# Performance work log

Hardware: AMD Instinct MI355X
Metric: run time of the kernel (lower is better)

The kernel has to match this reference:

```python
import jax, jax.numpy as jnp
import numpy as np

N_EMBD = 1024
N_HEAD = 16
HEAD_DIM = N_EMBD // N_HEAD
B, T = 2, 2048


def setup_inputs() -> dict:
    key = jax.random.key(0)
    ks = jax.random.split(key, 9)
    s = 1.0 / np.sqrt(N_EMBD)
    return {
        "x": jax.random.normal(ks[0], (B, T, N_EMBD), dtype=jnp.float32),
        "Wq": jax.random.normal(ks[1], (N_EMBD, N_EMBD), dtype=jnp.float32) * s,
        "bq": jax.random.normal(ks[2], (N_EMBD,), dtype=jnp.float32) * s,
        "Wk": jax.random.normal(ks[3], (N_EMBD, N_EMBD), dtype=jnp.float32) * s,
        "bk": jax.random.normal(ks[4], (N_EMBD,), dtype=jnp.float32) * s,
        "Wv": jax.random.normal(ks[5], (N_EMBD, N_EMBD), dtype=jnp.float32) * s,
        "bv": jax.random.normal(ks[6], (N_EMBD,), dtype=jnp.float32) * s,
        "Wp": jax.random.normal(ks[7], (N_EMBD, N_EMBD), dtype=jnp.float32) * s,
        "bp": jax.random.normal(ks[8], (N_EMBD,), dtype=jnp.float32) * s,
    }


def reference(x, Wq, bq, Wk, bk, Wv, bv, Wp, bp):
    b, t, c = x.shape
    # torch Linear: y = x @ W.T + b
    def proj(W, bias):
        y = jnp.einsum('btc,oc->bto', x, W) + bias
        return y.reshape(b, t, N_HEAD, HEAD_DIM).transpose(0, 2, 1, 3)  # [B,H,T,D]

    q = proj(Wq, bq)
    k = proj(Wk, bk)
    v = proj(Wv, bv)

    scale = 1.0 / np.sqrt(HEAD_DIM).astype(np.float32)
    scores = jnp.einsum('bhqd,bhkd->bhqk', q, k) * scale  # [B,H,T,T]
    causal = jnp.tril(jnp.ones((t, t), dtype=bool))
    scores = jnp.where(causal[None, None], scores, jnp.float32(-jnp.inf))
    attn = jax.nn.softmax(scores, axis=-1)
    out = jnp.einsum('bhqk,bhkd->bhqd', attn, v)  # [B,H,T,D]
    out = out.transpose(0, 2, 1, 3).reshape(b, t, c)
    out = jnp.einsum('btc,oc->bto', out, Wp) + bp
    return out
```

## Files before the change

kernel.cpp:

```cpp
#include <hip/hip_runtime.h>
#include <hip/hip_bf16.h>

#define TT 2048
#define MM 4096

typedef __attribute__((ext_vector_type(8))) short bf16x8;
typedef __attribute__((ext_vector_type(4))) float f32x4;

__device__ inline short f2bf(float f){
  union { float f; unsigned u; } x; x.f = f;
  unsigned r = x.u + 0x7FFFu + ((x.u >> 16) & 1u);
  return (short)(r >> 16);
}
__device__ inline int pk2bf(float a, float b){
  __hip_bfloat162 h2 = __float22bfloat162_rn(make_float2(a, b));
  return *(int*)&h2;
}

__device__ inline void async16(const void* g, void* l){
  __builtin_amdgcn_global_load_lds((const __attribute__((address_space(1))) void*)g,
                                   (__attribute__((address_space(3))) void*)l, 16, 0, 0);
}

__global__ void cvt_all(const float* __restrict__ x,
                        const float* __restrict__ Wq, const float* __restrict__ Wk,
                        const float* __restrict__ Wv, const float* __restrict__ Wp,
                        short* __restrict__ xb, short* __restrict__ Wqb, short* __restrict__ Wkb,
                        short* __restrict__ Wvb, short* __restrict__ Wpb){
  int b = blockIdx.x;
  const float* in; short* out; int base;
  if (b < 4096)      { in = x;  out = xb;  base = b; }
  else if (b < 5120) { in = Wq; out = Wqb; base = b - 4096; }
  else if (b < 6144) { in = Wk; out = Wkb; base = b - 5120; }
  else if (b < 7168) { in = Wv; out = Wvb; base = b - 6144; }
  else               { in = Wp; out = Wpb; base = b - 7168; }
  int i = base * 256 + threadIdx.x;
  float4 v = ((const float4*)in)[i];
  short4 o;
  o.x = f2bf(v.x); o.y = f2bf(v.y); o.z = f2bf(v.z); o.w = f2bf(v.w);
  ((short4*)out)[i] = o;
}

__device__ inline void gemm_core(const short* __restrict__ A, const short* __restrict__ Wm,
                                 short* As, short* Bs, int m0, int n0,
                                 int tid, int wm, int wn, int quad, int lr,
                                 f32x4 acc[4][4])
{
  const int prow = tid >> 2, pcol = (tid & 3) << 3;
  const short* Ap0 = A  + (size_t)(m0 + prow) * 1024 + pcol;
  const short* Ap1 = A  + (size_t)(m0 + prow + 64) * 1024 + pcol;
  const short* Bp0 = Wm + (size_t)(n0 + prow) * 1024 + pcol;
  const short* Bp1 = Wm + (size_t)(n0 + prow + 64) * 1024 + pcol;
  for (int kt = 0; kt < 16; ++kt){
    const int kk = kt * 64;
#pragma unroll
    for (int pn = 0; pn < 2; ++pn){
      async16(Ap0 + kk + pn*32, As + pn*4096 + (size_t)tid * 8);
      async16(Ap1 + kk + pn*32, As + pn*4096 + (size_t)(tid + 256) * 8);
      async16(Bp0 + kk + pn*32, Bs + pn*4096 + (size_t)tid * 8);
      async16(Bp1 + kk + pn*32, Bs + pn*4096 + (size_t)(tid + 256) * 8);
    }
    __syncthreads();
#pragma unroll
    for (int ks = 0; ks < 2; ++ks){
      bf16x8 aF[4], bF[4];
#pragma unroll
      for (int mt = 0; mt < 4; ++mt) aF[mt] = *(const bf16x8*)(As + ks*4096 + (wm*64 + mt*16 + lr)*32 + quad*8);
#pragma unroll
      for (int nt = 0; nt < 4; ++nt) bF[nt] = *(const bf16x8*)(Bs + ks*4096 + (wn*64 + nt*16 + lr)*32 + quad*8);
#pragma unroll
      for (int mt = 0; mt < 4; ++mt)
#pragma unroll
        for (int nt = 0; nt < 4; ++nt)
          acc[mt][nt] = __builtin_amdgcn_mfma_f32_16x16x32_bf16(aF[mt], bF[nt], acc[mt][nt], 0, 0, 0);
    }
    __syncthreads();
  }
}

__launch_bounds__(256, 3)
__global__ void gemm_qkv(const short* __restrict__ A,
                         const short* __restrict__ W0, const short* __restrict__ W1, const short* __restrict__ W2,
                         const float* __restrict__ b0, const float* __restrict__ b1, const float* __restrict__ b2,
                         short* __restrict__ Qo, short* __restrict__ Ko, short* __restrict__ Vt)
{
  __shared__ __align__(16) short smem[16384];
  short* As = smem;
  short* Bs = smem + 8192;
  const int z = blockIdx.z;
  const short* Wm   = (z == 0) ? W0 : ((z == 1) ? W1 : W2);
  const float* bias = (z == 0) ? b0 : ((z == 1) ? b1 : b2);
  const int tid = threadIdx.x;
  const int lane = tid & 63, wave = tid >> 6;
  const int wm = wave >> 1, wn = wave & 1;
  const int quad = lane >> 4, lr = lane & 15;
  const int m0 = blockIdx.y * 128, n0 = blockIdx.x * 128;

  f32x4 acc[4][4];
#pragma unroll
  for (int i = 0; i < 4; ++i)
#pragma unroll
    for (int j = 0; j < 4; ++j)
#pragma unroll
      for (int r = 0; r < 4; ++r) acc[i][j][r] = 0.f;

  gemm_core(A, Wm, As, Bs, m0, n0, tid, wm, wn, quad, lr, acc);

  const float qscale = 0.125f * 1.4426950408889634f;
  const int bB = m0 >> 11, t0 = m0 & 2047;

  if (z == 2){
#pragma unroll
    for (int nh = 0; nh < 2; ++nh){
      __syncthreads();
      if (wn == nh){
#pragma unroll
        for (int nt = 0; nt < 4; ++nt){
          int n = n0 + wn*64 + nt*16 + lr;
          float bv = bias[n];
          int n_l = nt*16 + lr;
#pragma unroll
          for (int mt = 0; mt < 4; ++mt)
#pragma unroll
            for (int r = 0; r < 4; ++r){
              int m_l = wm*64 + mt*16 + quad*4 + r;
              smem[n_l*136 + m_l] = f2bf(acc[mt][nt][r] + bv);
            }
        }
      }
      __syncthreads();
#pragma unroll
      for (int i = 0; i < 4; ++i){
        int c = tid + i*256;
        int rowN = c >> 4, ch = c & 15;
        int4 v = *(const int4*)(smem + rowN*136 + ch*8);
        int n = n0 + nh*64 + rowN;
        int hH = n >> 6, d = n & 63;
        *(int4*)(Vt + ((size_t)((bB<<4) + hH)*64 + d)*2048 + t0 + ch*8) = v;
      }
    }
    return;
  }

  short* dst = (z == 0) ? Qo : Ko;
#pragma unroll
  for (int nh = 0; nh < 2; ++nh){
    __syncthreads();
    if (wn == nh){
#pragma unroll
      for (int nt = 0; nt < 4; ++nt){
        int n_l = nt*16 + lr;
        float bv = bias[n0 + nh*64 + n_l];
#pragma unroll
        for (int mt = 0; mt < 4; ++mt){
#pragma unroll
          for (int r = 0; r < 4; ++r){
            int m_l = wm*64 + mt*16 + quad*4 + r;
            float v = acc[mt][nt][r] + bv;
            if (z == 0) v *= qscale;
            smem[m_l*72 + n_l] = f2bf(v);
          }
        }
      }
    }
    __syncthreads();
    const int hH = (n0 + nh*64) >> 6;
    short* dhead = dst + (size_t)((bB<<4) + hH) * 2048 * 64;
#pragma unroll
    for (int i = 0; i < 4; ++i){
      int c = tid + i*256;
      int rowm = c >> 3, ch = (c & 7) << 3;
      int4 v = *(const int4*)(smem + rowm*72 + ch);
      *(int4*)(dhead + (size_t)(t0 + rowm)*64 + ch) = v;
    }
  }
}

__launch_bounds__(256, 2)
__global__ void gemm_proj(const short* __restrict__ A, const short* __restrict__ Wm,
                          const float* __restrict__ bias, float* __restrict__ out)
{
  __shared__ __align__(16) short As[2*4096];
  __shared__ __align__(16) short Bs[2*2048];
  const int tid = threadIdx.x;
  const int lane = tid & 63, wave = tid >> 6;
  const int quad = lane >> 4, lr = lane & 15;
  const int m0 = blockIdx.y * 128, n0 = blockIdx.x * 64;

  const int prow = tid >> 2, pcol = (tid & 3) << 3;
  const short* Ap0 = A  + (size_t)(m0 + prow) * 1024 + pcol;
  const short* Ap1 = A  + (size_t)(m0 + prow + 64) * 1024 + pcol;
  const short* Bp0 = Wm + (size_t)(n0 + (tid >> 2)) * 1024 + pcol;

  f32x4 acc[2][4];
#pragma unroll
  for (int i = 0; i < 2; ++i)
#pragma unroll
    for (int j = 0; j < 4; ++j)
#pragma unroll
      for (int r = 0; r < 4; ++r) acc[i][j][r] = 0.f;

  for (int kt = 0; kt < 16; ++kt){
    const int kk = kt * 64;
#pragma unroll
    for (int pn = 0; pn < 2; ++pn){
      async16(Ap0 + kk + pn*32, As + pn*4096 + (size_t)tid * 8);
      async16(Ap1 + kk + pn*32, As + pn*4096 + (size_t)(tid + 256) * 8);
      async16(Bp0 + kk + pn*32, Bs + pn*2048 + (size_t)tid * 8);
    }
    __syncthreads();
#pragma unroll
    for (int ks = 0; ks < 2; ++ks){
      bf16x8 aF[2], bF[4];
#pragma unroll
      for (int mt = 0; mt < 2; ++mt) aF[mt] = *(const bf16x8*)(As + ks*4096 + (wave*32 + mt*16 + lr)*32 + quad*8);
#pragma unroll
      for (int nt = 0; nt < 4; ++nt) bF[nt] = *(const bf16x8*)(Bs + ks*2048 + (nt*16 + lr)*32 + quad*8);
#pragma unroll
      for (int mt = 0; mt < 2; ++mt)
#pragma unroll
        for (int nt = 0; nt < 4; ++nt)
          acc[mt][nt] = __builtin_amdgcn_mfma_f32_16x16x32_bf16(aF[mt], bF[nt], acc[mt][nt], 0, 0, 0);
    }
    __syncthreads();
  }

#pragma unroll
  for (int nt = 0; nt < 4; ++nt){
    int n = n0 + nt*16 + lr;
    float bv = bias[n];
#pragma unroll
    for (int mt = 0; mt < 2; ++mt){
      int mBase = m0 + wave*32 + mt*16 + quad*4;
#pragma unroll
      for (int r = 0; r < 4; ++r){
        int m = mBase + r;
        out[(size_t)m * 1024 + n] = acc[mt][nt][r] + bv;
      }
    }
  }
}

__launch_bounds__(256, 4)
__global__ void attn_kernel(const short* __restrict__ Q, const short* __restrict__ K,
                            const short* __restrict__ Vt, short* __restrict__ AO)
{
  __shared__ __align__(16) short Ks[2][4096];
  __shared__ __align__(16) short Vs[2][4096];
  __shared__ __align__(16) short Ps[4096];
  const int tid = threadIdx.x, lane = tid & 63, wave = tid >> 6;
  const int quad = lane >> 4, lr = lane & 15;
  const int bid = blockIdx.x;
  const int chunk = bid >> 8;
  const int a = (bid >> 5) & 7;
  int qt;
  if      (chunk == 0) qt = 31 - a;
  else if (chunk == 1) qt = a;
  else if (chunk == 2) qt = 23 - a;
  else                 qt = 8 + a;
  const int hb = bid & 31;
  const int bidx = hb >> 4, h = hb & 15;
  const int q0 = qt * 64;
  const int wq = q0 + wave * 16;
  const short* Qh = Q  + (size_t)hb * TT * 64;
  const short* Kh = K  + (size_t)hb * TT * 64;
  const short* Vh = Vt + (size_t)hb * 64 * TT;
  short* Pw = Ps + wave * 1024;

  const int srow = tid >> 3;
  const int ssw  = (tid & 7) ^ (srow & 7);
  const short* Kp0 = Kh + (size_t)srow * 64 + ssw * 8;
  const short* Vp0 = Vh + (size_t)srow * TT + ssw * 8;

  bf16x8 qf[2];
#pragma unroll
  for (int ks = 0; ks < 2; ++ks)
    qf[ks] = *(const bf16x8*)(Qh + (size_t)(wq + lr) * 64 + ks*32 + quad*8);

  const int lsw0 = (((0*4 + quad) ^ (lr & 7)) << 3);
  const int lsw1 = (((1*4 + quad) ^ (lr & 7)) << 3);
  const int qh2 = quad >> 1, qlo = (quad & 1) << 2;

  f32x4 acc_o[4], l_acc;
#pragma unroll
  for (int r = 0; r < 4; ++r) l_acc[r] = 0.f;
#pragma unroll
  for (int dt = 0; dt < 4; ++dt)
#pragma unroll
    for (int r = 0; r < 4; ++r) acc_o[dt][r] = 0.f;

  const short one_bf = (short)0x3F80;
  const bf16x8 onesf = { one_bf, one_bf, one_bf, one_bf, one_bf, one_bf, one_bf, one_bf };

  const int nkv = qt + 1;
  async16(Kp0,           &Ks[0][(size_t)tid * 8]);
  async16(Kp0 + 32*64,   &Ks[0][(size_t)(tid + 256) * 8]);
  async16(Vp0,           &Vs[0][(size_t)tid * 8]);
  async16(Vp0 + 32*TT,   &Vs[0][(size_t)(tid + 256) * 8]);

  int cur = 0;
  for (int kv = 0; kv < nkv; ++kv){
    const int kv0 = kv * 64;
    __syncthreads();
    if (kv + 1 < nkv){
      const short* kp = Kp0 + (size_t)(kv + 1) * 4096;
      const short* vp = Vp0 + (kv + 1) * 64;
      const int nb = cur ^ 1;
      async16(kp,          &Ks[nb][(size_t)tid * 8]);
      async16(kp + 32*64,  &Ks[nb][(size_t)(tid + 256) * 8]);
      async16(vp,          &Vs[nb][(size_t)tid * 8]);
      async16(vp + 32*TT,  &Vs[nb][(size_t)(tid + 256) * 8]);
    }
    if (kv0 <= wq + 15){
      f32x4 s4[4];
#pragma unroll
      for (int nt = 0; nt < 4; ++nt)
#pragma unroll
        for (int r = 0; r < 4; ++r) s4[nt][r] = 0.f;
#pragma unroll
      for (int nt = 0; nt < 4; ++nt){
        bf16x8 kf0 = *(const bf16x8*)(&Ks[cur][(nt*16 + lr)*64 + lsw0]);
        bf16x8 kf1 = *(const bf16x8*)(&Ks[cur][(nt*16 + lr)*64 + lsw1]);
        s4[nt] = __builtin_amdgcn_mfma_f32_16x16x32_bf16(kf0, qf[0], s4[nt], 0, 0, 0);
        s4[nt] = __builtin_amdgcn_mfma_f32_16x16x32_bf16(kf1, qf[1], s4[nt], 0, 0, 0);
      }

      const bool need_mask = (kv == nkv - 1);
      const int qglob = wq + lr;
#pragma unroll
      for (int nt = 0; nt < 4; ++nt){
        const int keyb = kv0 + nt*16 + quad*4;
        float pv[4];
#pragma unroll
        for (int r = 0; r < 4; ++r){
          float v = exp2f(s4[nt][r]);
          if (need_mask && keyb + r > qglob) v = 0.f;
          pv[r] = v;
        }
        int2 w;
        w.x = pk2bf(pv[0], pv[1]);
        w.y = pk2bf(pv[2], pv[3]);
        const int g = nt*2 + qh2;
        *(int2*)(Pw + lr*64 + ((g ^ (lr & 7)) << 3) + qlo) = w;
      }

#pragma unroll
      for (int ks = 0; ks < 2; ++ks){
        const int lsw = ks ? lsw1 : lsw0;
        bf16x8 ptf = *(const bf16x8*)(Pw + lr*64 + lsw);
        l_acc = __builtin_amdgcn_mfma_f32_16x16x32_bf16(onesf, ptf, l_acc, 0, 0, 0);
#pragma unroll
        for (int dt = 0; dt < 4; ++dt){
          bf16x8 vf = *(const bf16x8*)(&Vs[cur][(dt*16 + lr)*64 + lsw]);
          acc_o[dt] = __builtin_amdgcn_mfma_f32_16x16x32_bf16(vf, ptf, acc_o[dt], 0, 0, 0);
        }
      }
    }
    cur ^= 1;
  }

  const float inv = __builtin_amdgcn_rcpf(l_acc[0]);
#pragma unroll
  for (int dt = 0; dt < 4; ++dt){
    int2 w;
    w.x = pk2bf(acc_o[dt][0] * inv, acc_o[dt][1] * inv);
    w.y = pk2bf(acc_o[dt][2] * inv, acc_o[dt][3] * inv);
    const int g = dt*2 + qh2;
    *(int2*)(Pw + lr*64 + ((g ^ (lr & 7)) << 3) + qlo) = w;
  }
#pragma unroll
  for (int i = 0; i < 2; ++i){
    int c = lane + i*64;
    int row = c >> 3, ch = c & 7;
    int4 v = *(const int4*)(Pw + row*64 + ((ch ^ (row & 7)) << 3));
    *(int4*)(AO + (size_t)(bidx*2048 + wq + row)*1024 + h*64 + ch*8) = v;
  }
}

extern "C" void kernel_launch(void* const* d_in, const int* in_sizes, int n_in,
                              void* d_out, int out_size, void* d_ws, size_t ws_size,
                              hipStream_t stream)
{
  const float* x  = (const float*)d_in[0];
  const float* Wq = (const float*)d_in[1];
  const float* bq = (const float*)d_in[2];
  const float* Wk = (const float*)d_in[3];
  const float* bk = (const float*)d_in[4];
  const float* Wv = (const float*)d_in[5];
  const float* bv = (const float*)d_in[6];
  const float* Wp = (const float*)d_in[7];
  const float* bp = (const float*)d_in[8];
  float* out = (float*)d_out;

  char* ws = (char*)d_ws;
  const size_t MB = 1024ull * 1024ull;
  short* Qb  = (short*)(ws + 0);
  short* Kb  = (short*)(ws + 8*MB);
  short* Vtb = (short*)(ws + 16*MB);
  short* AOb = (short*)(ws + 24*MB);
  short* xb  = (short*)(ws + 24*MB);
  short* Wqb = (short*)(ws + 32*MB);
  short* Wkb = (short*)(ws + 34*MB);
  short* Wvb = (short*)(ws + 36*MB);
  short* Wpb = (short*)(ws + 38*MB);

  cvt_all<<<8192, 256, 0, stream>>>(x, Wq, Wk, Wv, Wp, xb, Wqb, Wkb, Wvb, Wpb);
  gemm_qkv<<<dim3(8, 32, 3), 256, 0, stream>>>(xb, Wqb, Wkb, Wvb, bq, bk, bv, Qb, Kb, Vtb);
  attn_kernel<<<1024, 256, 0, stream>>>(Qb, Kb, Vtb, AOb);
  gemm_proj<<<dim3(16, 32), 256, 0, stream>>>(AOb, Wpb, bp, out);
}
```

Baseline: 180.5 us.

## Load K fragments directly from global into registers with register prefetch

Drops the shared-memory double buffer for K and has each wave load its K MFMA fragments straight from global memory into registers. The next tile's fragments are prefetched into a second register set after the QK^T MFMAs. This removes LDS traffic and LDS capacity for K, which may allow more blocks per CU. The cost is that all four waves now read the same K tile separately from global/L2, and the extra 16 vector registers per lane raise register pressure.

```diff
diff --git a/kernel.cpp b/kernel.cpp
--- a/kernel.cpp
+++ b/kernel.cpp
@@ -245,7 +245,6 @@
 __global__ void attn_kernel(const short* __restrict__ Q, const short* __restrict__ K,
                             const short* __restrict__ Vt, short* __restrict__ AO)
 {
-  __shared__ __align__(16) short Ks[2][4096];
   __shared__ __align__(16) short Vs[2][4096];
   __shared__ __align__(16) short Ps[4096];
   const int tid = threadIdx.x, lane = tid & 63, wave = tid >> 6;
@@ -269,8 +268,9 @@
 
   const int srow = tid >> 3;
   const int ssw  = (tid & 7) ^ (srow & 7);
-  const short* Kp0 = Kh + (size_t)srow * 64 + ssw * 8;
   const short* Vp0 = Vh + (size_t)srow * TT + ssw * 8;
+
+  const short* Kf0 = Kh + (size_t)lr * 64 + quad * 8;
 
   bf16x8 qf[2];
 #pragma unroll
@@ -293,21 +293,23 @@
   const bf16x8 onesf = { one_bf, one_bf, one_bf, one_bf, one_bf, one_bf, one_bf, one_bf };
 
   const int nkv = qt + 1;
-  async16(Kp0,           &Ks[0][(size_t)tid * 8]);
-  async16(Kp0 + 32*64,   &Ks[0][(size_t)(tid + 256) * 8]);
-  async16(Vp0,           &Vs[0][(size_t)tid * 8]);
-  async16(Vp0 + 32*TT,   &Vs[0][(size_t)(tid + 256) * 8]);
+  async16(Vp0,         &Vs[0][(size_t)tid * 8]);
+  async16(Vp0 + 32*TT, &Vs[0][(size_t)(tid + 256) * 8]);
+  bf16x8 kf[4][2], kn[4][2];
+#pragma unroll
+  for (int nt = 0; nt < 4; ++nt)
+#pragma unroll
+    for (int ks = 0; ks < 2; ++ks)
+      kf[nt][ks] = *(const bf16x8*)(Kf0 + nt*16*64 + ks*32);
 
   int cur = 0;
   for (int kv = 0; kv < nkv; ++kv){
     const int kv0 = kv * 64;
     __syncthreads();
-    if (kv + 1 < nkv){
-      const short* kp = Kp0 + (size_t)(kv + 1) * 4096;
+    const bool more = (kv + 1 < nkv);
+    if (more){
       const short* vp = Vp0 + (kv + 1) * 64;
       const int nb = cur ^ 1;
-      async16(kp,          &Ks[nb][(size_t)tid * 8]);
-      async16(kp + 32*64,  &Ks[nb][(size_t)(tid + 256) * 8]);
       async16(vp,          &Vs[nb][(size_t)tid * 8]);
       async16(vp + 32*TT,  &Vs[nb][(size_t)(tid + 256) * 8]);
     }
@@ -319,10 +321,17 @@
         for (int r = 0; r < 4; ++r) s4[nt][r] = 0.f;
 #pragma unroll
       for (int nt = 0; nt < 4; ++nt){
-        bf16x8 kf0 = *(const bf16x8*)(&Ks[cur][(nt*16 + lr)*64 + lsw0]);
-        bf16x8 kf1 = *(const bf16x8*)(&Ks[cur][(nt*16 + lr)*64 + lsw1]);
-        s4[nt] = __builtin_amdgcn_mfma_f32_16x16x32_bf16(kf0, qf[0], s4[nt], 0, 0, 0);
-        s4[nt] = __builtin_amdgcn_mfma_f32_16x16x32_bf16(kf1, qf[1], s4[nt], 0, 0, 0);
+        s4[nt] = __builtin_amdgcn_mfma_f32_16x16x32_bf16(kf[nt][0], qf[0], s4[nt], 0, 0, 0);
+        s4[nt] = __builtin_amdgcn_mfma_f32_16x16x32_bf16(kf[nt][1], qf[1], s4[nt], 0, 0, 0);
+      }
+
+      if (more){
+        const short* kp = Kf0 + (size_t)(kv + 1) * 4096;
+#pragma unroll
+        for (int nt = 0; nt < 4; ++nt)
+#pragma unroll
+          for (int ks = 0; ks < 2; ++ks)
+            kn[nt][ks] = *(const bf16x8*)(kp + nt*16*64 + ks*32);
       }
 
       const bool need_mask = (kv == nkv - 1);
@@ -355,7 +364,19 @@
           acc_o[dt] = __builtin_amdgcn_mfma_f32_16x16x32_bf16(vf, ptf, acc_o[dt], 0, 0, 0);
         }
       }
-    }
+    } else if (more){
+      const short* kp = Kf0 + (size_t)(kv + 1) * 4096;
+#pragma unroll
+      for (int nt = 0; nt < 4; ++nt)
+#pragma unroll
+        for (int ks = 0; ks < 2; ++ks)
+          kn[nt][ks] = *(const bf16x8*)(kp + nt*16*64 + ks*32);
+    }
+#pragma unroll
+    for (int nt = 0; nt < 4; ++nt)
+#pragma unroll
+      for (int ks = 0; ks < 2; ++ks)
+        kf[nt][ks] = kn[nt][ks];
     cur ^= 1;
   }
 
```

After: 214.8 us. +19.1%, slower.

## Double-buffer LDS tiles in QKV and projection GEMMs to overlap loads with MFMA

Applied to the files above, without the earlier changes.

Both GEMM main loops now use two 32-wide K buffers in LDS. The next K slice is issued with async global-to-LDS loads before the MFMAs run on the current slice, replacing the old load-everything, sync, compute, sync pattern. The aim is to hide global memory latency behind matrix math and drop one barrier per step. In exchange there are twice as many loop iterations, each doing less work, and correctness depends on the barrier at the top of each iteration also waiting for the outstanding async loads.

```diff
diff --git a/kernel.cpp b/kernel.cpp
--- a/kernel.cpp
+++ b/kernel.cpp
@@ -51,30 +51,32 @@
   const short* Ap1 = A  + (size_t)(m0 + prow + 64) * 1024 + pcol;
   const short* Bp0 = Wm + (size_t)(n0 + prow) * 1024 + pcol;
   const short* Bp1 = Wm + (size_t)(n0 + prow + 64) * 1024 + pcol;
-  for (int kt = 0; kt < 16; ++kt){
-    const int kk = kt * 64;
-#pragma unroll
-    for (int pn = 0; pn < 2; ++pn){
-      async16(Ap0 + kk + pn*32, As + pn*4096 + (size_t)tid * 8);
-      async16(Ap1 + kk + pn*32, As + pn*4096 + (size_t)(tid + 256) * 8);
-      async16(Bp0 + kk + pn*32, Bs + pn*4096 + (size_t)tid * 8);
-      async16(Bp1 + kk + pn*32, Bs + pn*4096 + (size_t)(tid + 256) * 8);
-    }
+  async16(Ap0, As + (size_t)tid * 8);
+  async16(Ap1, As + (size_t)(tid + 256) * 8);
+  async16(Bp0, Bs + (size_t)tid * 8);
+  async16(Bp1, Bs + (size_t)(tid + 256) * 8);
+  int cur = 0;
+  for (int kt = 0; kt < 32; ++kt){
     __syncthreads();
-#pragma unroll
-    for (int ks = 0; ks < 2; ++ks){
-      bf16x8 aF[4], bF[4];
-#pragma unroll
-      for (int mt = 0; mt < 4; ++mt) aF[mt] = *(const bf16x8*)(As + ks*4096 + (wm*64 + mt*16 + lr)*32 + quad*8);
-#pragma unroll
-      for (int nt = 0; nt < 4; ++nt) bF[nt] = *(const bf16x8*)(Bs + ks*4096 + (wn*64 + nt*16 + lr)*32 + quad*8);
-#pragma unroll
-      for (int mt = 0; mt < 4; ++mt)
-#pragma unroll
-        for (int nt = 0; nt < 4; ++nt)
-          acc[mt][nt] = __builtin_amdgcn_mfma_f32_16x16x32_bf16(aF[mt], bF[nt], acc[mt][nt], 0, 0, 0);
-    }
-    __syncthreads();
+    if (kt + 1 < 32){
+      const int kk = (kt + 1) * 32;
+      const int nb = cur ^ 1;
+      async16(Ap0 + kk, As + nb*4096 + (size_t)tid * 8);
+      async16(Ap1 + kk, As + nb*4096 + (size_t)(tid + 256) * 8);
+      async16(Bp0 + kk, Bs + nb*4096 + (size_t)tid * 8);
+      async16(Bp1 + kk, Bs + nb*4096 + (size_t)(tid + 256) * 8);
+    }
+    bf16x8 aF[4], bF[4];
+#pragma unroll
+    for (int mt = 0; mt < 4; ++mt) aF[mt] = *(const bf16x8*)(As + cur*4096 + (wm*64 + mt*16 + lr)*32 + quad*8);
+#pragma unroll
+    for (int nt = 0; nt < 4; ++nt) bF[nt] = *(const bf16x8*)(Bs + cur*4096 + (wn*64 + nt*16 + lr)*32 + quad*8);
+#pragma unroll
+    for (int mt = 0; mt < 4; ++mt)
+#pragma unroll
+      for (int nt = 0; nt < 4; ++nt)
+        acc[mt][nt] = __builtin_amdgcn_mfma_f32_16x16x32_bf16(aF[mt], bF[nt], acc[mt][nt], 0, 0, 0);
+    cur ^= 1;
   }
 }
 
@@ -190,7 +192,7 @@
   const int prow = tid >> 2, pcol = (tid & 3) << 3;
   const short* Ap0 = A  + (size_t)(m0 + prow) * 1024 + pcol;
   const short* Ap1 = A  + (size_t)(m0 + prow + 64) * 1024 + pcol;
-  const short* Bp0 = Wm + (size_t)(n0 + (tid >> 2)) * 1024 + pcol;
+  const short* Bp0 = Wm + (size_t)(n0 + prow) * 1024 + pcol;
 
   f32x4 acc[2][4];
 #pragma unroll
@@ -200,29 +202,30 @@
 #pragma unroll
       for (int r = 0; r < 4; ++r) acc[i][j][r] = 0.f;
 
-  for (int kt = 0; kt < 16; ++kt){
-    const int kk = kt * 64;
-#pragma unroll
-    for (int pn = 0; pn < 2; ++pn){
-      async16(Ap0 + kk + pn*32, As + pn*4096 + (size_t)tid * 8);
-      async16(Ap1 + kk + pn*32, As + pn*4096 + (size_t)(tid + 256) * 8);
-      async16(Bp0 + kk + pn*32, Bs + pn*2048 + (size_t)tid * 8);
-    }
+  async16(Ap0, As + (size_t)tid * 8);
+  async16(Ap1, As + (size_t)(tid + 256) * 8);
+  async16(Bp0, Bs + (size_t)tid * 8);
+  int cur = 0;
+  for (int kt = 0; kt < 32; ++kt){
     __syncthreads();
-#pragma unroll
-    for (int ks = 0; ks < 2; ++ks){
-      bf16x8 aF[2], bF[4];
-#pragma unroll
-      for (int mt = 0; mt < 2; ++mt) aF[mt] = *(const bf16x8*)(As + ks*4096 + (wave*32 + mt*16 + lr)*32 + quad*8);
-#pragma unroll
-      for (int nt = 0; nt < 4; ++nt) bF[nt] = *(const bf16x8*)(Bs + ks*2048 + (nt*16 + lr)*32 + quad*8);
-#pragma unroll
-      for (int mt = 0; mt < 2; ++mt)
-#pragma unroll
-        for (int nt = 0; nt < 4; ++nt)
-          acc[mt][nt] = __builtin_amdgcn_mfma_f32_16x16x32_bf16(aF[mt], bF[nt], acc[mt][nt], 0, 0, 0);
-    }
-    __syncthreads();
+    if (kt + 1 < 32){
+      const int kk = (kt + 1) * 32;
+      const int nb = cur ^ 1;
+      async16(Ap0 + kk, As + nb*4096 + (size_t)tid * 8);
+      async16(Ap1 + kk, As + nb*4096 + (size_t)(tid + 256) * 8);
+      async16(Bp0 + kk, Bs + nb*2048 + (size_t)tid * 8);
+    }
+    bf16x8 aF[2], bF[4];
+#pragma unroll
+    for (int mt = 0; mt < 2; ++mt) aF[mt] = *(const bf16x8*)(As + cur*4096 + (wave*32 + mt*16 + lr)*32 + quad*8);
+#pragma unroll
+    for (int nt = 0; nt < 4; ++nt) bF[nt] = *(const bf16x8*)(Bs + cur*2048 + (nt*16 + lr)*32 + quad*8);
+#pragma unroll
+    for (int mt = 0; mt < 2; ++mt)
+#pragma unroll
+      for (int nt = 0; nt < 4; ++nt)
+        acc[mt][nt] = __builtin_amdgcn_mfma_f32_16x16x32_bf16(aF[mt], bF[nt], acc[mt][nt], 0, 0, 0);
+    cur ^= 1;
   }
 
 #pragma unroll
```

Measured after the change: 181.4 us. About the same (+0.5%).
